# Kernel tuning notes

Hardware: AMD Instinct MI355X
Metric: run time of the kernel (lower is better)

Reference implementation:

```python
import jax, jax.numpy as jnp
import numpy as np

N_HEADS = 28
N_KV_HEADS = 4
HEAD_DIM = 128
ROPE_THETA = 1000000.0


def _sinusoidal_positions(num_pos, dim, theta):
    # Mirrors create_sinusoidal_positions: interleaved [sin, cos] pairs -> (num_pos, dim)
    positions = jnp.arange(0, num_pos, dtype=jnp.float32)
    half_dim = dim // 2
    freq_indices = jnp.arange(0, half_dim, dtype=jnp.float32)
    inv_freq = 1.0 / theta ** (freq_indices / half_dim)
    sinusoid_inp = jnp.einsum('i,j->ij', positions, inv_freq)
    return jnp.stack([jnp.sin(sinusoid_inp), jnp.cos(sinusoid_inp)], axis=-1).reshape(num_pos, -1)


def _rotate_half(x):
    x1, x2 = jnp.split(x, 2, axis=-1)
    return jnp.concatenate([-x2, x1], axis=-1)


def _apply_rope(q, k, sinu_pos):
    # Mirrors apply_rotary_pos_emb: split halves, duplicate, rotate_half mixing.
    sin, cos = jnp.split(sinu_pos, 2, axis=-1)
    sin = jnp.concatenate([sin, sin], axis=-1)[None, None, :, :]
    cos = jnp.concatenate([cos, cos], axis=-1)[None, None, :, :]
    q_embed = q * cos + _rotate_half(q) * sin
    k_embed = k * cos + _rotate_half(k) * sin
    return q_embed, k_embed


def setup_inputs() -> dict:
    key = jax.random.key(0)
    ks = jax.random.split(key, 5)
    B, S, H = 2, 2048, 3584
    std = 0.02
    return {
        'hidden_states': jax.random.normal(ks[0], (B, S, H), dtype=jnp.float32),
        'wq': jax.random.normal(ks[1], (H, N_HEADS * HEAD_DIM), dtype=jnp.float32) * std,
        'wk': jax.random.normal(ks[2], (H, N_KV_HEADS * HEAD_DIM), dtype=jnp.float32) * std,
        'wv': jax.random.normal(ks[3], (H, N_KV_HEADS * HEAD_DIM), dtype=jnp.float32) * std,
        'wo': jax.random.normal(ks[4], (N_HEADS * HEAD_DIM, H), dtype=jnp.float32) * std,
    }


def reference(hidden_states, wq, wk, wv, wo):
    B, S, H = hidden_states.shape
    gqa_ratio = N_HEADS // N_KV_HEADS

    # QKV projections (bias-free) and head split -> (B, heads, S, d)
    q = (hidden_states @ wq).reshape(B, S, N_HEADS, HEAD_DIM).transpose(0, 2, 1, 3)
    k = (hidden_states @ wk).reshape(B, S, N_KV_HEADS, HEAD_DIM).transpose(0, 2, 1, 3)
    v = (hidden_states @ wv).reshape(B, S, N_KV_HEADS, HEAD_DIM).transpose(0, 2, 1, 3)

    # Inline RoPE on Q/K
    sincos = _sinusoidal_positions(S, HEAD_DIM, ROPE_THETA)
    q, k = _apply_rope(q, k, sincos)

    # GQA head expansion via tile (matches jnp.tile in source: block-repeat)
    k = jnp.tile(k, (1, gqa_ratio, 1, 1))
    v = jnp.tile(v, (1, gqa_ratio, 1, 1))

    # Causal scaled dot-product attention
    scale = 1.0 / jnp.sqrt(jnp.float32(HEAD_DIM))
    scores = jnp.einsum('bhqd,bhkd->bhqk', q, k) * scale  # (B, H, S, S)
    causal = jnp.tril(jnp.ones((S, S), dtype=bool))
    scores = jnp.where(causal[None, None], scores, jnp.finfo(scores.dtype).min)
    probs = jax.nn.softmax(scores, axis=-1)
    out = jnp.einsum('bhqk,bhkd->bhqd', probs, v)

    # Merge heads and output projection
    out = out.transpose(0, 2, 1, 3).reshape(B, S, N_HEADS * HEAD_DIM)
    return out @ wo
```

## Files before the change

### kernel.cpp

```cpp
#include <hip/hip_runtime.h>
#include <hip/hip_bf16.h>

typedef __attribute__((ext_vector_type(4))) float f32x4;
typedef __attribute__((ext_vector_type(8))) short s16x8;
typedef __attribute__((ext_vector_type(4))) short s16x4;
typedef unsigned short u16;

__device__ __forceinline__ u16 f2bf(float f) {
  union { float f; unsigned int u; } v; v.f = f;
  unsigned int r = v.u + 0x7fffu + ((v.u >> 16) & 1u);
  return (u16)(r >> 16);
}
__device__ __forceinline__ float bf2f(u16 x) {
  union { unsigned u; float f; } v; v.u = ((unsigned)x) << 16; return v.f;
}

__device__ __forceinline__ void gload_lds16(const void* g, void* l) {
  __builtin_amdgcn_global_load_lds(
      (const __attribute__((address_space(1))) void*)g,
      (__attribute__((address_space(3))) void*)l, 16, 0, 0);
}

__global__ __launch_bounds__(256) void cvt_bf16(const float* __restrict__ in,
                                                u16* __restrict__ outp, int nquad) {
  int i = blockIdx.x * 256 + threadIdx.x;
  if (i >= nquad) return;
  f32x4 v = *(const f32x4*)(in + (size_t)i * 4);
  s16x4 o;
  o.x = (short)f2bf(v.x); o.y = (short)f2bf(v.y);
  o.z = (short)f2bf(v.z); o.w = (short)f2bf(v.w);
  *(s16x4*)(outp + (size_t)i * 4) = o;
}

__global__ __launch_bounds__(256) void transpose_cvt(const float* __restrict__ in,
                                                     u16* __restrict__ outp, int R, int C) {
  __shared__ float t[32][33];
  int c0 = blockIdx.x * 32, r0 = blockIdx.y * 32;
  int tx = threadIdx.x & 31, ty = threadIdx.x >> 5;
#pragma unroll
  for (int i = 0; i < 32; i += 8) t[ty + i][tx] = in[(size_t)(r0 + ty + i) * C + c0 + tx];
  __syncthreads();
#pragma unroll
  for (int i = 0; i < 32; i += 8)
    outp[(size_t)(c0 + ty + i) * R + r0 + tx] = f2bf(t[tx][ty + i]);
}

__global__ void rope_table(float2* __restrict__ tab) {
  int p = blockIdx.x, e = threadIdx.x;
  int j = e >> 1;
  float f1 = powf(1.0e6f, -(float)j / 64.0f);
  float f2 = powf(1.0e6f, -(float)(j + 32) / 64.0f);
  float a1 = (float)p * f1, a2 = (float)p * f2;
  float S = (e & 1) ? cosf(a1) : sinf(a1);
  float C = (e & 1) ? cosf(a2) : sinf(a2);
  tab[p * 64 + e] = make_float2(S, C);
}

__global__ __launch_bounds__(256) void rope_pack(const u16* __restrict__ P,
                                                 const float2* __restrict__ tab,
                                                 u16* __restrict__ outp, int nh, int ldp,
                                                 int coff, float scale) {
  int idx = blockIdx.x * 4 + (threadIdx.x >> 6);
  int e = threadIdx.x & 63;
  int s = idx & 2047;
  int bh = idx >> 11;
  int b = bh / nh, h = bh - b * nh;
  size_t prow = ((size_t)(b * 2048 + s)) * (size_t)ldp + coff + (size_t)h * 128;
  float x1 = bf2f(P[prow + e]), x2 = bf2f(P[prow + e + 64]);
  float2 t = tab[s * 64 + e];
  float o1 = (x1 * t.y - x2 * t.x) * scale;
  float o2 = (x2 * t.y + x1 * t.x) * scale;
  size_t orow = (size_t)idx * 128;
  outp[orow + e] = f2bf(o1);
  outp[orow + e + 64] = f2bf(o2);
}

__global__ __launch_bounds__(256) void pack_vt(const u16* __restrict__ P,
                                               u16* __restrict__ Vt, int ldp, int coff) {
  __shared__ u16 t[32][33];
  int bk = blockIdx.z;
  int b = bk >> 2, kh = bk & 3;
  int s0 = blockIdx.x * 32, d0 = blockIdx.y * 32;
  int tx = threadIdx.x & 31, ty = threadIdx.x >> 5;
  const u16* in = P + (size_t)(b * 2048) * ldp + coff + kh * 128;
#pragma unroll
  for (int i = 0; i < 32; i += 8) t[ty + i][tx] = in[(size_t)(s0 + ty + i) * ldp + d0 + tx];
  __syncthreads();
  u16* outp = Vt + (size_t)bk * 128 * 2048;
#pragma unroll
  for (int i = 0; i < 32; i += 8)
    outp[(size_t)(d0 + ty + i) * 2048 + s0 + tx] = t[tx][ty + i];
}

template <int OUT_BF16>
__global__ __launch_bounds__(512, 2) void gemm256(const u16* __restrict__ A,
                                                  const u16* __restrict__ BT,
                                                  void* __restrict__ Cv,
                                                  int M, int N, int K) {
  extern __shared__ u16 sm[];
  const int tid = threadIdx.x;
  const int lane = tid & 63, w = tid >> 6;
  const int wm = w >> 2, wn = w & 3;
  const int r = lane & 15, g = lane >> 4;
  const int bm = blockIdx.y * 256, bn = blockIdx.x * 256;

  f32x4 acc[8][4];
#pragma unroll
  for (int mf = 0; mf < 8; mf++)
#pragma unroll
    for (int nf = 0; nf < 4; nf++) acc[mf][nf] = (f32x4){0.f, 0.f, 0.f, 0.f};

  const int row_s = tid >> 3;
  const int col_s = ((((tid & 7) << 4) ^ ((row_s & 7) << 4)) >> 1);
  const u16* sAg[4]; const u16* sBg[4];
#pragma unroll
  for (int i = 0; i < 4; i++) {
    sAg[i] = A  + (size_t)(bm + i * 64 + row_s) * K + col_s;
    sBg[i] = BT + (size_t)(bn + i * 64 + row_s) * K + col_s;
  }

#pragma unroll
  for (int i = 0; i < 4; i++) gload_lds16(sAg[i], sm + i * 4096 + w * 512);
#pragma unroll
  for (int i = 0; i < 4; i++) gload_lds16(sBg[i], sm + 32768 + i * 4096 + w * 512);

  const int NT = K >> 6;
  const int swz = (r & 7) << 4;
#pragma unroll 1
  for (int t = 0; t < NT; ++t) {
    const int p = t & 1;
    const u16* LA = sm + p * 16384;
    const u16* LB = sm + 32768 + p * 16384;
    u16* SA = sm + (p ^ 1) * 16384;
    u16* SB = sm + 32768 + (p ^ 1) * 16384;
    const int ktn = (t + 1 < NT) ? (t + 1) * 64 : 0;

    __builtin_amdgcn_s_barrier();
    gload_lds16(sAg[0] + ktn, SA + 0 * 4096 + w * 512);
    gload_lds16(sAg[1] + ktn, SA + 1 * 4096 + w * 512);
    asm volatile("s_waitcnt vmcnt(2)" ::: "memory");
    __builtin_amdgcn_s_barrier();
    __builtin_amdgcn_sched_barrier(0);

    const char* Ac = (const char*)LA;
    const char* Bc = (const char*)LB;
    s16x8 bf[4][2];
#pragma unroll
    for (int nf = 0; nf < 4; nf++)
#pragma unroll
      for (int ks = 0; ks < 2; ks++) {
        int row = wn * 64 + nf * 16 + r;
        bf[nf][ks] = *(const s16x8*)(Bc + ((row * 128 + ks * 64 + g * 16) ^ swz));
      }
#pragma unroll
    for (int ph = 0; ph < 4; ph++) {
      if (ph == 1) {
        gload_lds16(sAg[2] + ktn, SA + 2 * 4096 + w * 512);
        gload_lds16(sAg[3] + ktn, SA + 3 * 4096 + w * 512);
      } else if (ph == 2) {
        gload_lds16(sBg[0] + ktn, SB + 0 * 4096 + w * 512);
        gload_lds16(sBg[1] + ktn, SB + 1 * 4096 + w * 512);
      } else if (ph == 3) {
        gload_lds16(sBg[2] + ktn, SB + 2 * 4096 + w * 512);
        gload_lds16(sBg[3] + ktn, SB + 3 * 4096 + w * 512);
      }
      s16x8 af[2][2];
#pragma unroll
      for (int mi = 0; mi < 2; mi++)
#pragma unroll
        for (int ks = 0; ks < 2; ks++) {
          int row = wm * 128 + (ph * 2 + mi) * 16 + r;
          af[mi][ks] = *(const s16x8*)(Ac + ((row * 128 + ks * 64 + g * 16) ^ swz));
        }
      __builtin_amdgcn_s_setprio(1);
#pragma unroll
      for (int mi = 0; mi < 2; mi++)
#pragma unroll
        for (int nf = 0; nf < 4; nf++) {
          acc[ph * 2 + mi][nf] = __builtin_amdgcn_mfma_f32_16x16x32_bf16(
              af[mi][0], bf[nf][0], acc[ph * 2 + mi][nf], 0, 0, 0);
          acc[ph * 2 + mi][nf] = __builtin_amdgcn_mfma_f32_16x16x32_bf16(
              af[mi][1], bf[nf][1], acc[ph * 2 + mi][nf], 0, 0, 0);
        }
      __builtin_amdgcn_s_setprio(0);
    }
  }
  asm volatile("s_waitcnt vmcnt(0)" ::: "memory");

#pragma unroll
  for (int mf = 0; mf < 8; mf++)
#pragma unroll
    for (int nf = 0; nf < 4; nf++)
#pragma unroll
      for (int jj = 0; jj < 4; jj++) {
        size_t idx = (size_t)(bm + wm * 128 + mf * 16 + g * 4 + jj) * N +
                     (bn + wn * 64 + nf * 16 + r);
        if constexpr (OUT_BF16) ((u16*)Cv)[idx] = f2bf(acc[mf][nf][jj]);
        else                    ((float*)Cv)[idx] = acc[mf][nf][jj];
      }
}

__global__ __launch_bounds__(256, 4) void attn_kernel(const u16* __restrict__ Q,
                                                      const u16* __restrict__ K,
                                                      const u16* __restrict__ Vt,
                                                      u16* __restrict__ AO) {
  constexpr int S = 2048, NH = 28, NKV = 4, D = 128;
  __shared__ u16 Kl[2][32 * 128];
  __shared__ u16 Vl[2][32 * 128];
  const int tid = threadIdx.x;
  const int lane = tid & 63, w = tid >> 6;
  const int r = lane & 15, g = lane >> 4;
  const int pp = blockIdx.x, h = blockIdx.y, b = blockIdx.z;
  const int kh = h & 3;
  const u16* Kb = K + ((size_t)(b * NKV + kh) * S) * D;
  const u16* Vb = Vt + ((size_t)(b * NKV + kh) * D) * S;

  const u16 *sK[2], *sV[2];
#pragma unroll
  for (int i = 0; i < 2; i++) {
    int o = i * 4096 + tid * 16;
    int krow = o >> 8;
    int kcol = ((o & 255) ^ ((krow & 7) << 4)) >> 1;
    sK[i] = Kb + (size_t)krow * D + kcol;
    int p = o ^ (((o >> 7) & 7) << 4);
    sV[i] = Vb + (size_t)(p >> 6) * S + ((p & 63) >> 1);
  }

#pragma unroll 1
  for (int seg = 0; seg < 2; ++seg) {
    const int qt = seg ? (31 - pp) : pp;
    const int q0 = qt * 64 + w * 16;
    const u16* Qb = Q + ((size_t)(b * NH + h) * S + q0) * D;

    s16x8 qf[4];
#pragma unroll
    for (int kb = 0; kb < 4; kb++)
      qf[kb] = *(const s16x8*)(Qb + (size_t)r * D + kb * 32 + g * 8);

    f32x4 o8[8];
#pragma unroll
    for (int c = 0; c < 8; c++) o8[c] = (f32x4){0.f, 0.f, 0.f, 0.f};
    float m = -1e30f, lsum = 0.f;
    const int qg = q0 + r;
    const int NT = 2 * qt + 2;

#pragma unroll
    for (int i = 0; i < 2; i++) {
      gload_lds16(sK[i], (u16*)Kl[0] + i * 2048 + tid * 8);
      gload_lds16(sV[i], (u16*)Vl[0] + i * 2048 + tid * 8);
    }

    int cur = 0;
#pragma unroll 1
    for (int t = 0; t < NT; ++t) {
      const int j = t * 32;
      if (t + 1 < NT) {
        const size_t jn = (size_t)(j + 32);
#pragma unroll
        for (int i = 0; i < 2; i++) {
          gload_lds16(sK[i] + jn * D, (u16*)Kl[cur ^ 1] + i * 2048 + tid * 8);
          gload_lds16(sV[i] + jn,     (u16*)Vl[cur ^ 1] + i * 2048 + tid * 8);
        }
        asm volatile("s_waitcnt vmcnt(4)" ::: "memory");
      } else {
        asm volatile("s_waitcnt vmcnt(0)" ::: "memory");
      }
      __builtin_amdgcn_s_barrier();
      __builtin_amdgcn_sched_barrier(0);
      if (j <= q0 + 15) {
        f32x4 st0 = (f32x4){0.f, 0.f, 0.f, 0.f};
        f32x4 st1 = (f32x4){0.f, 0.f, 0.f, 0.f};
        const int swz = (r & 7) << 4;
        const char* Kc = (const char*)Kl[cur];
        __builtin_amdgcn_s_setprio(1);
#pragma unroll
        for (int kb = 0; kb < 4; kb++) {
          int cb = (kb * 64 + g * 16) ^ swz;
          s16x8 kf = *(const s16x8*)(Kc + r * 256 + cb);
          st0 = __builtin_amdgcn_mfma_f32_16x16x32_bf16(kf, qf[kb], st0, 0, 0, 0);
        }
#pragma unroll
        for (int kb = 0; kb < 4; kb++) {
          int cb = (kb * 64 + g * 16) ^ swz;
          s16x8 kf = *(const s16x8*)(Kc + (r + 16) * 256 + cb);
          st1 = __builtin_amdgcn_mfma_f32_16x16x32_bf16(kf, qf[kb], st1, 0, 0, 0);
        }
        __builtin_amdgcn_s_setprio(0);
        float s8v[8];
        if (j + 31 <= q0) {
#pragma unroll
          for (int jj = 0; jj < 4; jj++) { s8v[jj] = st0[jj]; s8v[jj + 4] = st1[jj]; }
        } else {
#pragma unroll
          for (int jj = 0; jj < 4; jj++) {
            int kv0 = j + g * 4 + jj;
            s8v[jj] = (kv0 > qg) ? -1e30f : st0[jj];
            s8v[jj + 4] = (kv0 + 16 > qg) ? -1e30f : st1[jj];
          }
        }
        float pm = fmaxf(fmaxf(fmaxf(s8v[0], s8v[1]), fmaxf(s8v[2], s8v[3])),
                         fmaxf(fmaxf(s8v[4], s8v[5]), fmaxf(s8v[6], s8v[7])));
        const bool defer = __all(pm <= m + 8.f);
        float fr = 1.f;
        if (!defer) {
          pm = fmaxf(pm, __shfl_xor(pm, 16));
          pm = fmaxf(pm, __shfl_xor(pm, 32));
          float mnew = fmaxf(m, pm);
          fr = __expf(m - mnew);
          m = mnew;
        }
        float pv[8], psum = 0.f;
#pragma unroll
        for (int i2 = 0; i2 < 8; i2++) { pv[i2] = __expf(s8v[i2] - m); psum += pv[i2]; }
        lsum = lsum * fr + psum;
        unsigned pk[4];
#pragma unroll
        for (int i2 = 0; i2 < 4; i2++) {
          __hip_bfloat162 hv = __float22bfloat162_rn(make_float2(pv[2 * i2], pv[2 * i2 + 1]));
          union { __hip_bfloat162 h; unsigned u; } cv; cv.h = hv; pk[i2] = cv.u;
        }
        int L0 = r + ((g & 1) << 5);
        unsigned a0 = (unsigned)__shfl((int)pk[0], L0);
        unsigned a1 = (unsigned)__shfl((int)pk[1], L0);
        unsigned a2 = (unsigned)__shfl((int)pk[2], L0);
        unsigned a3 = (unsigned)__shfl((int)pk[3], L0);
        unsigned b0 = (unsigned)__shfl((int)pk[0], L0 + 16);
        unsigned b1 = (unsigned)__shfl((int)pk[1], L0 + 16);
        unsigned b2 = (unsigned)__shfl((int)pk[2], L0 + 16);
        unsigned b3 = (unsigned)__shfl((int)pk[3], L0 + 16);
        union { unsigned u[4]; s16x8 v; } pu;
        pu.u[0] = (g < 2) ? a0 : a2;
        pu.u[1] = (g < 2) ? a1 : a3;
        pu.u[2] = (g < 2) ? b0 : b2;
        pu.u[3] = (g < 2) ? b1 : b3;
        s16x8 pa = pu.v;
        float fB[4];
        if (!defer) {
#pragma unroll
          for (int jj = 0; jj < 4; jj++) fB[jj] = __shfl(fr, g * 4 + jj);
        }
        const char* Vc = (const char*)Vl[cur];
        __builtin_amdgcn_s_setprio(1);
#pragma unroll
        for (int c = 0; c < 8; c++) {
          int pbyte = (c * 16 + r) * 64 + g * 16;
          int vaddr = pbyte ^ ((r >> 1) << 4);
          s16x8 vf = *(const s16x8*)(Vc + vaddr);
          f32x4 oc = o8[c];
          if (!defer) { oc.x *= fB[0]; oc.y *= fB[1]; oc.z *= fB[2]; oc.w *= fB[3]; }
          o8[c] = __builtin_amdgcn_mfma_f32_16x16x32_bf16(pa, vf, oc, 0, 0, 0);
        }
        __builtin_amdgcn_s_setprio(0);
      }
      __builtin_amdgcn_s_barrier();
      cur ^= 1;
    }

    float lrow = lsum;
    lrow += __shfl_xor(lrow, 16);
    lrow += __shfl_xor(lrow, 32);
    float lB[4];
#pragma unroll
    for (int jj = 0; jj < 4; jj++) lB[jj] = __shfl(lrow, g * 4 + jj);
#pragma unroll
    for (int c = 0; c < 8; c++)
#pragma unroll
      for (int jj = 0; jj < 4; jj++) {
        float val = o8[c][jj] / lB[jj];
        AO[(size_t)(b * S + q0 + g * 4 + jj) * 3584 + h * 128 + c * 16 + r] = f2bf(val);
      }
  }
}

static const size_t OFF_XBF = 0;
static const size_t OFF_WQT = 29360128;
static const size_t OFF_WKT = 55050240;
static const size_t OFF_WVT = 58720256;
static const size_t OFF_WOT = 62390272;
static const size_t OFF_TAB = 88080384;
static const size_t OFF_QBF = 89128960;
static const size_t OFF_KBF = 118489088;
static const size_t OFF_VT  = 122683392;
static const size_t OFF_QKV = 126877696;
static const size_t OFF_AO  = 164626432;

extern "C" void kernel_launch(void* const* d_in, const int* in_sizes, int n_in,
                              void* d_out, int out_size, void* d_ws, size_t ws_size,
                              hipStream_t stream) {
  const float* X  = (const float*)d_in[0];
  const float* Wq = (const float*)d_in[1];
  const float* Wk = (const float*)d_in[2];
  const float* Wv = (const float*)d_in[3];
  const float* Wo = (const float*)d_in[4];
  float* out = (float*)d_out;
  char* ws = (char*)d_ws;

  u16* Xbf = (u16*)(ws + OFF_XBF);
  u16* WqT = (u16*)(ws + OFF_WQT);
  u16* WkT = (u16*)(ws + OFF_WKT);
  u16* WvT = (u16*)(ws + OFF_WVT);
  u16* WoT = (u16*)(ws + OFF_WOT);
  float2* tab = (float2*)(ws + OFF_TAB);
  u16* Qbf = (u16*)(ws + OFF_QBF);
  u16* Kbf = (u16*)(ws + OFF_KBF);
  u16* Vtb = (u16*)(ws + OFF_VT);
  u16* QKV = (u16*)(ws + OFF_QKV);
  u16* AO  = (u16*)(ws + OFF_AO);

  hipFuncSetAttribute(reinterpret_cast<const void*>(gemm256<1>),
                      hipFuncAttributeMaxDynamicSharedMemorySize, 131072);
  hipFuncSetAttribute(reinterpret_cast<const void*>(gemm256<0>),
                      hipFuncAttributeMaxDynamicSharedMemorySize, 131072);

  cvt_bf16<<<14336, 256, 0, stream>>>(X, Xbf, 3670016);
  transpose_cvt<<<dim3(112, 112), 256, 0, stream>>>(Wq, WqT, 3584, 3584);
  transpose_cvt<<<dim3(16, 112), 256, 0, stream>>>(Wk, WkT, 3584, 512);
  transpose_cvt<<<dim3(16, 112), 256, 0, stream>>>(Wv, WvT, 3584, 512);
  transpose_cvt<<<dim3(112, 112), 256, 0, stream>>>(Wo, WoT, 3584, 3584);
  rope_table<<<2048, 64, 0, stream>>>(tab);

  gemm256<1><<<dim3(18, 16), 512, 131072, stream>>>(Xbf, WqT, QKV, 4096, 4608, 3584);

  rope_pack<<<28672, 256, 0, stream>>>(QKV, tab, Qbf, 28, 4608, 0, 0.08838834764831845f);
  rope_pack<<<4096, 256, 0, stream>>>(QKV, tab, Kbf, 4, 4608, 3584, 1.0f);
  pack_vt<<<dim3(64, 4, 8), 256, 0, stream>>>(QKV, Vtb, 4608, 4096);

  attn_kernel<<<dim3(16, 28, 2), 256, 0, stream>>>(Qbf, Kbf, Vtb, AO);

  gemm256<0><<<dim3(14, 16), 512, 131072, stream>>>(AO, WoT, out, 4096, 3584, 3584);
}
```

Measured before the change: 510.2 us.

## Deepen GEMM prefetch to two stages and remap tiles per XCD

The 256x256 bf16 GEMM is restructured to prefetch the K-tile two iterations ahead, loading into the LDS buffer currently being consumed. Barriers are placed around each MFMA phase so loads can overwrite parts of the buffer once they have been read. Block IDs are also remapped so that blocks landing on the same XCD cover a contiguous rectangle of output tiles, which is meant to improve L2 reuse of A and B. The extra barriers per phase add synchronisation cost, and the in-place buffer reuse depends on the barrier placement being correct.

New measurement: 522.7 us. 1.02x slower.

```diff
diff --git a/kernel.cpp b/kernel.cpp
--- a/kernel.cpp
+++ b/kernel.cpp
@@ -96,13 +96,17 @@
 __global__ __launch_bounds__(512, 2) void gemm256(const u16* __restrict__ A,
                                                   const u16* __restrict__ BT,
                                                   void* __restrict__ Cv,
-                                                  int M, int N, int K) {
+                                                  int M, int N, int K,
+                                                  int CNX, int CNY, int XNX) {
   extern __shared__ u16 sm[];
   const int tid = threadIdx.x;
   const int lane = tid & 63, w = tid >> 6;
   const int wm = w >> 2, wn = w & 3;
   const int r = lane & 15, g = lane >> 4;
-  const int bm = blockIdx.y * 256, bn = blockIdx.x * 256;
+  const int lid = blockIdx.x;
+  const int xcd = lid & 7, pos = lid >> 3;
+  const int bn = ((xcd % XNX) * CNX + pos % CNX) * 256;
+  const int bm = ((xcd / XNX) * CNY + pos / CNX) * 256;
 
   f32x4 acc[8][4];
 #pragma unroll
@@ -120,49 +124,51 @@
   }
 
 #pragma unroll
-  for (int i = 0; i < 4; i++) gload_lds16(sAg[i], sm + i * 4096 + w * 512);
-#pragma unroll
   for (int i = 0; i < 4; i++) gload_lds16(sBg[i], sm + 32768 + i * 4096 + w * 512);
+  gload_lds16(sAg[0], sm + 0 * 4096 + w * 512);
+  gload_lds16(sAg[2], sm + 2 * 4096 + w * 512);
+  gload_lds16(sAg[1], sm + 1 * 4096 + w * 512);
+  gload_lds16(sAg[3], sm + 3 * 4096 + w * 512);
+#pragma unroll
+  for (int i = 0; i < 4; i++) gload_lds16(sBg[i] + 64, sm + 49152 + i * 4096 + w * 512);
+  gload_lds16(sAg[0] + 64, sm + 16384 + 0 * 4096 + w * 512);
+  gload_lds16(sAg[2] + 64, sm + 16384 + 2 * 4096 + w * 512);
+  gload_lds16(sAg[1] + 64, sm + 16384 + 1 * 4096 + w * 512);
+  gload_lds16(sAg[3] + 64, sm + 16384 + 3 * 4096 + w * 512);
+  asm volatile("s_waitcnt vmcnt(8)" ::: "memory");
+  __builtin_amdgcn_s_barrier();
 
   const int NT = K >> 6;
   const int swz = (r & 7) << 4;
 #pragma unroll 1
   for (int t = 0; t < NT; ++t) {
     const int p = t & 1;
-    const u16* LA = sm + p * 16384;
-    const u16* LB = sm + 32768 + p * 16384;
-    u16* SA = sm + (p ^ 1) * 16384;
-    u16* SB = sm + 32768 + (p ^ 1) * 16384;
-    const int ktn = (t + 1 < NT) ? (t + 1) * 64 : 0;
-
-    __builtin_amdgcn_s_barrier();
-    gload_lds16(sAg[0] + ktn, SA + 0 * 4096 + w * 512);
-    gload_lds16(sAg[1] + ktn, SA + 1 * 4096 + w * 512);
-    asm volatile("s_waitcnt vmcnt(2)" ::: "memory");
-    __builtin_amdgcn_s_barrier();
-    __builtin_amdgcn_sched_barrier(0);
-
-    const char* Ac = (const char*)LA;
-    const char* Bc = (const char*)LB;
+    const char* Ac = (const char*)(sm + p * 16384);
+    const char* Bc = (const char*)(sm + 32768 + p * 16384);
+    u16* SA = sm + p * 16384;
+    u16* SB = sm + 32768 + p * 16384;
+    const int kt2 = (t + 2 < NT) ? (t + 2) * 64 : 0;
+
     s16x8 bf[4][2];
-#pragma unroll
-    for (int nf = 0; nf < 4; nf++)
-#pragma unroll
-      for (int ks = 0; ks < 2; ks++) {
-        int row = wn * 64 + nf * 16 + r;
-        bf[nf][ks] = *(const s16x8*)(Bc + ((row * 128 + ks * 64 + g * 16) ^ swz));
-      }
 #pragma unroll
     for (int ph = 0; ph < 4; ph++) {
       if (ph == 1) {
-        gload_lds16(sAg[2] + ktn, SA + 2 * 4096 + w * 512);
-        gload_lds16(sAg[3] + ktn, SA + 3 * 4096 + w * 512);
+        gload_lds16(sBg[0] + kt2, SB + 0 * 4096 + w * 512);
+        gload_lds16(sBg[1] + kt2, SB + 1 * 4096 + w * 512);
+        gload_lds16(sBg[2] + kt2, SB + 2 * 4096 + w * 512);
+        gload_lds16(sBg[3] + kt2, SB + 3 * 4096 + w * 512);
       } else if (ph == 2) {
-        gload_lds16(sBg[0] + ktn, SB + 0 * 4096 + w * 512);
-        gload_lds16(sBg[1] + ktn, SB + 1 * 4096 + w * 512);
-      } else if (ph == 3) {
-        gload_lds16(sBg[2] + ktn, SB + 2 * 4096 + w * 512);
-        gload_lds16(sBg[3] + ktn, SB + 3 * 4096 + w * 512);
+        gload_lds16(sAg[0] + kt2, SA + 0 * 4096 + w * 512);
+        gload_lds16(sAg[2] + kt2, SA + 2 * 4096 + w * 512);
+      }
+      if (ph == 0) {
+#pragma unroll
+        for (int nf = 0; nf < 4; nf++)
+#pragma unroll
+          for (int ks = 0; ks < 2; ks++) {
+            int row = wn * 64 + nf * 16 + r;
+            bf[nf][ks] = *(const s16x8*)(Bc + ((row * 128 + ks * 64 + g * 16) ^ swz));
+          }
       }
       s16x8 af[2][2];
 #pragma unroll
@@ -172,6 +178,8 @@
           int row = wm * 128 + (ph * 2 + mi) * 16 + r;
           af[mi][ks] = *(const s16x8*)(Ac + ((row * 128 + ks * 64 + g * 16) ^ swz));
         }
+      __builtin_amdgcn_s_barrier();
+      __builtin_amdgcn_sched_barrier(0);
       __builtin_amdgcn_s_setprio(1);
 #pragma unroll
       for (int mi = 0; mi < 2; mi++)
@@ -183,7 +191,14 @@
               af[mi][1], bf[nf][1], acc[ph * 2 + mi][nf], 0, 0, 0);
         }
       __builtin_amdgcn_s_setprio(0);
+      __builtin_amdgcn_s_barrier();
+      __builtin_amdgcn_sched_barrier(0);
     }
+    gload_lds16(sAg[1] + kt2, SA + 1 * 4096 + w * 512);
+    gload_lds16(sAg[3] + kt2, SA + 3 * 4096 + w * 512);
+    asm volatile("s_waitcnt vmcnt(8)" ::: "memory");
+    __builtin_amdgcn_s_barrier();
+    __builtin_amdgcn_sched_barrier(0);
   }
   asm volatile("s_waitcnt vmcnt(0)" ::: "memory");
 
@@ -419,7 +434,7 @@
   transpose_cvt<<<dim3(112, 112), 256, 0, stream>>>(Wo, WoT, 3584, 3584);
   rope_table<<<2048, 64, 0, stream>>>(tab);
 
-  gemm256<1><<<dim3(18, 16), 512, 131072, stream>>>(Xbf, WqT, QKV, 4096, 4608, 3584);
+  gemm256<1><<<288, 512, 131072, stream>>>(Xbf, WqT, QKV, 4096, 4608, 3584, 9, 4, 2);
 
   rope_pack<<<28672, 256, 0, stream>>>(QKV, tab, Qbf, 28, 4608, 0, 0.08838834764831845f);
   rope_pack<<<4096, 256, 0, stream>>>(QKV, tab, Kbf, 4, 4608, 3584, 1.0f);
@@ -427,5 +442,5 @@
 
   attn_kernel<<<dim3(16, 28, 2), 256, 0, stream>>>(Qbf, Kbf, Vtb, AO);
 
-  gemm256<0><<<dim3(14, 16), 512, 131072, stream>>>(AO, WoT, out, 4096, 3584, 3584);
-}
+  gemm256<0><<<224, 512, 131072, stream>>>(AO, WoT, out, 4096, 3584, 3584, 7, 4, 2);
+}
```

## Remap GEMM tiles per XCD and restructure double-buffered load pipeline

Applied to the files above, without the earlier changes.

Switches the GEMM grid to a 1D launch and maps block IDs so that each of the 8 XCDs gets a contiguous rectangular group of output tiles, which should improve L2 reuse of A and B panels. The K-loop prefetch is reordered so B tiles load first and A tiles later. Explicit vmcnt waits and barriers now bracket each MFMA phase, replacing the single barrier pair at the top of each iteration. This adds more barriers per iteration, and the mapping assumes round-robin dispatch of blocks across XCDs.

Result: slower. 521.0 us (+2.1%).

```diff
diff --git a/kernel.cpp b/kernel.cpp
--- a/kernel.cpp
+++ b/kernel.cpp
@@ -96,13 +96,17 @@
 __global__ __launch_bounds__(512, 2) void gemm256(const u16* __restrict__ A,
                                                   const u16* __restrict__ BT,
                                                   void* __restrict__ Cv,
-                                                  int M, int N, int K) {
+                                                  int M, int N, int K,
+                                                  int CNX, int CNY, int XNX) {
   extern __shared__ u16 sm[];
   const int tid = threadIdx.x;
   const int lane = tid & 63, w = tid >> 6;
   const int wm = w >> 2, wn = w & 3;
   const int r = lane & 15, g = lane >> 4;
-  const int bm = blockIdx.y * 256, bn = blockIdx.x * 256;
+  const int lid = blockIdx.x;
+  const int xcd = lid & 7, pos = lid >> 3;
+  const int bn = ((xcd % XNX) * CNX + pos % CNX) * 256;
+  const int bm = ((xcd / XNX) * CNY + pos / CNX) * 256;
 
   f32x4 acc[8][4];
 #pragma unroll
@@ -120,49 +124,51 @@
   }
 
 #pragma unroll
-  for (int i = 0; i < 4; i++) gload_lds16(sAg[i], sm + i * 4096 + w * 512);
-#pragma unroll
   for (int i = 0; i < 4; i++) gload_lds16(sBg[i], sm + 32768 + i * 4096 + w * 512);
+  gload_lds16(sAg[0], sm + 0 * 4096 + w * 512);
+  gload_lds16(sAg[2], sm + 2 * 4096 + w * 512);
+  gload_lds16(sAg[1], sm + 1 * 4096 + w * 512);
+  gload_lds16(sAg[3], sm + 3 * 4096 + w * 512);
+  asm volatile("s_waitcnt vmcnt(2)" ::: "memory");
+  __builtin_amdgcn_s_barrier();
 
   const int NT = K >> 6;
   const int swz = (r & 7) << 4;
 #pragma unroll 1
   for (int t = 0; t < NT; ++t) {
     const int p = t & 1;
-    const u16* LA = sm + p * 16384;
-    const u16* LB = sm + 32768 + p * 16384;
+    const char* Ac = (const char*)(sm + p * 16384);
+    const char* Bc = (const char*)(sm + 32768 + p * 16384);
     u16* SA = sm + (p ^ 1) * 16384;
     u16* SB = sm + 32768 + (p ^ 1) * 16384;
     const int ktn = (t + 1 < NT) ? (t + 1) * 64 : 0;
 
-    __builtin_amdgcn_s_barrier();
-    gload_lds16(sAg[0] + ktn, SA + 0 * 4096 + w * 512);
-    gload_lds16(sAg[1] + ktn, SA + 1 * 4096 + w * 512);
-    asm volatile("s_waitcnt vmcnt(2)" ::: "memory");
-    __builtin_amdgcn_s_barrier();
-    __builtin_amdgcn_sched_barrier(0);
-
-    const char* Ac = (const char*)LA;
-    const char* Bc = (const char*)LB;
     s16x8 bf[4][2];
 #pragma unroll
-    for (int nf = 0; nf < 4; nf++)
-#pragma unroll
-      for (int ks = 0; ks < 2; ks++) {
-        int row = wn * 64 + nf * 16 + r;
-        bf[nf][ks] = *(const s16x8*)(Bc + ((row * 128 + ks * 64 + g * 16) ^ swz));
-      }
-#pragma unroll
     for (int ph = 0; ph < 4; ph++) {
-      if (ph == 1) {
-        gload_lds16(sAg[2] + ktn, SA + 2 * 4096 + w * 512);
-        gload_lds16(sAg[3] + ktn, SA + 3 * 4096 + w * 512);
-      } else if (ph == 2) {
+      if (ph == 0) {
         gload_lds16(sBg[0] + ktn, SB + 0 * 4096 + w * 512);
         gload_lds16(sBg[1] + ktn, SB + 1 * 4096 + w * 512);
-      } else if (ph == 3) {
+      } else if (ph == 1) {
         gload_lds16(sBg[2] + ktn, SB + 2 * 4096 + w * 512);
         gload_lds16(sBg[3] + ktn, SB + 3 * 4096 + w * 512);
+        asm volatile("s_waitcnt vmcnt(4)" ::: "memory");
+      } else if (ph == 2) {
+        gload_lds16(sAg[0] + ktn, SA + 0 * 4096 + w * 512);
+        gload_lds16(sAg[2] + ktn, SA + 2 * 4096 + w * 512);
+      } else {
+        gload_lds16(sAg[1] + ktn, SA + 1 * 4096 + w * 512);
+        gload_lds16(sAg[3] + ktn, SA + 3 * 4096 + w * 512);
+        asm volatile("s_waitcnt vmcnt(2)" ::: "memory");
+      }
+      if (ph == 0) {
+#pragma unroll
+        for (int nf = 0; nf < 4; nf++)
+#pragma unroll
+          for (int ks = 0; ks < 2; ks++) {
+            int row = wn * 64 + nf * 16 + r;
+            bf[nf][ks] = *(const s16x8*)(Bc + ((row * 128 + ks * 64 + g * 16) ^ swz));
+          }
       }
       s16x8 af[2][2];
 #pragma unroll
@@ -172,6 +178,7 @@
           int row = wm * 128 + (ph * 2 + mi) * 16 + r;
           af[mi][ks] = *(const s16x8*)(Ac + ((row * 128 + ks * 64 + g * 16) ^ swz));
         }
+      __builtin_amdgcn_s_barrier();
       __builtin_amdgcn_s_setprio(1);
 #pragma unroll
       for (int mi = 0; mi < 2; mi++)
@@ -183,6 +190,7 @@
               af[mi][1], bf[nf][1], acc[ph * 2 + mi][nf], 0, 0, 0);
         }
       __builtin_amdgcn_s_setprio(0);
+      __builtin_amdgcn_s_barrier();
     }
   }
   asm volatile("s_waitcnt vmcnt(0)" ::: "memory");
@@ -419,7 +427,7 @@
   transpose_cvt<<<dim3(112, 112), 256, 0, stream>>>(Wo, WoT, 3584, 3584);
   rope_table<<<2048, 64, 0, stream>>>(tab);
 
-  gemm256<1><<<dim3(18, 16), 512, 131072, stream>>>(Xbf, WqT, QKV, 4096, 4608, 3584);
+  gemm256<1><<<288, 512, 131072, stream>>>(Xbf, WqT, QKV, 4096, 4608, 3584, 9, 4, 2);
 
   rope_pack<<<28672, 256, 0, stream>>>(QKV, tab, Qbf, 28, 4608, 0, 0.08838834764831845f);
   rope_pack<<<4096, 256, 0, stream>>>(QKV, tab, Kbf, 4, 4608, 3584, 1.0f);
@@ -427,5 +435,5 @@
 
   attn_kernel<<<dim3(16, 28, 2), 256, 0, stream>>>(Qbf, Kbf, Vtb, AO);
 
-  gemm256<0><<<dim3(14, 16), 512, 131072, stream>>>(AO, WoT, out, 4096, 3584, 3584);
-}
+  gemm256<0><<<224, 512, 131072, stream>>>(AO, WoT, out, 4096, 3584, 3584, 7, 4, 2);
+}
```

## Replace 256x256 GEMM with 128x128 tile kernel for better CU fill

Applied to the files above, without the earlier changes.

Swaps the 512-thread, 256x256-tile GEMM (128KB dynamic LDS, K-step 64) for a 256-thread 128x128-tile kernel with 32KB static LDS, a K-step of 32 and a simple double buffer. Both the QKV and output projections now launch several times as many blocks. This is meant to fix poor wave quantisation: the output projection previously ran only 224 blocks on a 256-CU device. The cost is less data reuse per tile, more global and LDS traffic, and more barriers per K-iteration. The attention output buffer now reuses the QKV workspace region.

Result: slower. 550.2 us (+7.8%).

```diff
diff --git a/kernel.cpp b/kernel.cpp
--- a/kernel.cpp
+++ b/kernel.cpp
@@ -92,111 +92,87 @@
     outp[(size_t)(d0 + ty + i) * 2048 + s0 + tx] = t[tx][ty + i];
 }
 
-template <int OUT_BF16>
-__global__ __launch_bounds__(512, 2) void gemm256(const u16* __restrict__ A,
+__global__ __launch_bounds__(256, 3) void gemm128(const u16* __restrict__ A,
                                                   const u16* __restrict__ BT,
                                                   void* __restrict__ Cv,
-                                                  int M, int N, int K) {
-  extern __shared__ u16 sm[];
+                                                  int M, int N, int K, int obf16) {
+  __shared__ u16 sm[16384];
   const int tid = threadIdx.x;
-  const int lane = tid & 63, w = tid >> 6;
-  const int wm = w >> 2, wn = w & 3;
+  const int lane = tid & 63, wave = tid >> 6;
+  const int bm = blockIdx.y * 128, bn = blockIdx.x * 128;
+  const int wr = (wave >> 1) * 64, wc = (wave & 1) * 64;
   const int r = lane & 15, g = lane >> 4;
-  const int bm = blockIdx.y * 256, bn = blockIdx.x * 256;
-
-  f32x4 acc[8][4];
-#pragma unroll
-  for (int mf = 0; mf < 8; mf++)
-#pragma unroll
-    for (int nf = 0; nf < 4; nf++) acc[mf][nf] = (f32x4){0.f, 0.f, 0.f, 0.f};
-
-  const int row_s = tid >> 3;
-  const int col_s = ((((tid & 7) << 4) ^ ((row_s & 7) << 4)) >> 1);
-  const u16* sAg[4]; const u16* sBg[4];
-#pragma unroll
-  for (int i = 0; i < 4; i++) {
-    sAg[i] = A  + (size_t)(bm + i * 64 + row_s) * K + col_s;
-    sBg[i] = BT + (size_t)(bn + i * 64 + row_s) * K + col_s;
+
+  f32x4 acc[4][4];
+#pragma unroll
+  for (int i = 0; i < 4; i++)
+#pragma unroll
+    for (int j = 0; j < 4; j++) acc[i][j] = (f32x4){0.f, 0.f, 0.f, 0.f};
+
+  const u16 *srcA[2], *srcB[2];
+#pragma unroll
+  for (int i = 0; i < 2; i++) {
+    int row = i * 64 + (tid >> 2);
+    int cb = ((tid & 3) * 16) ^ (((row >> 1) & 3) << 4);
+    srcA[i] = A  + (size_t)(bm + row) * K + (cb >> 1);
+    srcB[i] = BT + (size_t)(bn + row) * K + (cb >> 1);
   }
 
 #pragma unroll
-  for (int i = 0; i < 4; i++) gload_lds16(sAg[i], sm + i * 4096 + w * 512);
-#pragma unroll
-  for (int i = 0; i < 4; i++) gload_lds16(sBg[i], sm + 32768 + i * 4096 + w * 512);
-
-  const int NT = K >> 6;
-  const int swz = (r & 7) << 4;
+  for (int i = 0; i < 2; i++) gload_lds16(srcA[i], sm + i * 2048 + tid * 8);
+#pragma unroll
+  for (int i = 0; i < 2; i++) gload_lds16(srcB[i], sm + 8192 + i * 2048 + tid * 8);
+
+  const int NT = K >> 5;
 #pragma unroll 1
   for (int t = 0; t < NT; ++t) {
     const int p = t & 1;
-    const u16* LA = sm + p * 16384;
-    const u16* LB = sm + 32768 + p * 16384;
-    u16* SA = sm + (p ^ 1) * 16384;
-    u16* SB = sm + 32768 + (p ^ 1) * 16384;
-    const int ktn = (t + 1 < NT) ? (t + 1) * 64 : 0;
-
+    const char* Ac = (const char*)(sm + p * 4096);
+    const char* Bc = (const char*)(sm + 8192 + p * 4096);
+    if (t + 1 < NT) {
+      const int ktn = (t + 1) * 32;
+      u16* SA = sm + (p ^ 1) * 4096;
+      u16* SB = sm + 8192 + (p ^ 1) * 4096;
+#pragma unroll
+      for (int i = 0; i < 2; i++) gload_lds16(srcA[i] + ktn, SA + i * 2048 + tid * 8);
+#pragma unroll
+      for (int i = 0; i < 2; i++) gload_lds16(srcB[i] + ktn, SB + i * 2048 + tid * 8);
+      asm volatile("s_waitcnt vmcnt(4)" ::: "memory");
+    } else {
+      asm volatile("s_waitcnt vmcnt(0)" ::: "memory");
+    }
     __builtin_amdgcn_s_barrier();
-    gload_lds16(sAg[0] + ktn, SA + 0 * 4096 + w * 512);
-    gload_lds16(sAg[1] + ktn, SA + 1 * 4096 + w * 512);
-    asm volatile("s_waitcnt vmcnt(2)" ::: "memory");
+
+    s16x8 af[4], bf[4];
+#pragma unroll
+    for (int mf = 0; mf < 4; mf++) {
+      int row = wr + mf * 16 + r;
+      af[mf] = *(const s16x8*)(Ac + row * 64 + ((g * 16) ^ (((row >> 1) & 3) << 4)));
+    }
+#pragma unroll
+    for (int nf = 0; nf < 4; nf++) {
+      int row = wc + nf * 16 + r;
+      bf[nf] = *(const s16x8*)(Bc + row * 64 + ((g * 16) ^ (((row >> 1) & 3) << 4)));
+    }
+    __builtin_amdgcn_s_setprio(1);
+#pragma unroll
+    for (int mf = 0; mf < 4; mf++)
+#pragma unroll
+      for (int nf = 0; nf < 4; nf++)
+        acc[mf][nf] = __builtin_amdgcn_mfma_f32_16x16x32_bf16(af[mf], bf[nf], acc[mf][nf], 0, 0, 0);
+    __builtin_amdgcn_s_setprio(0);
     __builtin_amdgcn_s_barrier();
-    __builtin_amdgcn_sched_barrier(0);
-
-    const char* Ac = (const char*)LA;
-    const char* Bc = (const char*)LB;
-    s16x8 bf[4][2];
+  }
+
+#pragma unroll
+  for (int mf = 0; mf < 4; mf++)
 #pragma unroll
     for (int nf = 0; nf < 4; nf++)
 #pragma unroll
-      for (int ks = 0; ks < 2; ks++) {
-        int row = wn * 64 + nf * 16 + r;
-        bf[nf][ks] = *(const s16x8*)(Bc + ((row * 128 + ks * 64 + g * 16) ^ swz));
-      }
-#pragma unroll
-    for (int ph = 0; ph < 4; ph++) {
-      if (ph == 1) {
-        gload_lds16(sAg[2] + ktn, SA + 2 * 4096 + w * 512);
-        gload_lds16(sAg[3] + ktn, SA + 3 * 4096 + w * 512);
-      } else if (ph == 2) {
-        gload_lds16(sBg[0] + ktn, SB + 0 * 4096 + w * 512);
-        gload_lds16(sBg[1] + ktn, SB + 1 * 4096 + w * 512);
-      } else if (ph == 3) {
-        gload_lds16(sBg[2] + ktn, SB + 2 * 4096 + w * 512);
-        gload_lds16(sBg[3] + ktn, SB + 3 * 4096 + w * 512);
-      }
-      s16x8 af[2][2];
-#pragma unroll
-      for (int mi = 0; mi < 2; mi++)
-#pragma unroll
-        for (int ks = 0; ks < 2; ks++) {
-          int row = wm * 128 + (ph * 2 + mi) * 16 + r;
-          af[mi][ks] = *(const s16x8*)(Ac + ((row * 128 + ks * 64 + g * 16) ^ swz));
-        }
-      __builtin_amdgcn_s_setprio(1);
-#pragma unroll
-      for (int mi = 0; mi < 2; mi++)
-#pragma unroll
-        for (int nf = 0; nf < 4; nf++) {
-          acc[ph * 2 + mi][nf] = __builtin_amdgcn_mfma_f32_16x16x32_bf16(
-              af[mi][0], bf[nf][0], acc[ph * 2 + mi][nf], 0, 0, 0);
-          acc[ph * 2 + mi][nf] = __builtin_amdgcn_mfma_f32_16x16x32_bf16(
-              af[mi][1], bf[nf][1], acc[ph * 2 + mi][nf], 0, 0, 0);
-        }
-      __builtin_amdgcn_s_setprio(0);
-    }
-  }
-  asm volatile("s_waitcnt vmcnt(0)" ::: "memory");
-
-#pragma unroll
-  for (int mf = 0; mf < 8; mf++)
-#pragma unroll
-    for (int nf = 0; nf < 4; nf++)
-#pragma unroll
       for (int jj = 0; jj < 4; jj++) {
-        size_t idx = (size_t)(bm + wm * 128 + mf * 16 + g * 4 + jj) * N +
-                     (bn + wn * 64 + nf * 16 + r);
-        if constexpr (OUT_BF16) ((u16*)Cv)[idx] = f2bf(acc[mf][nf][jj]);
-        else                    ((float*)Cv)[idx] = acc[mf][nf][jj];
+        size_t idx = (size_t)(bm + wr + mf * 16 + g * 4 + jj) * N + (bn + wc + nf * 16 + r);
+        if (obf16) ((u16*)Cv)[idx] = f2bf(acc[mf][nf][jj]);
+        else       ((float*)Cv)[idx] = acc[mf][nf][jj];
       }
 }
 
@@ -382,7 +358,6 @@
 static const size_t OFF_KBF = 118489088;
 static const size_t OFF_VT  = 122683392;
 static const size_t OFF_QKV = 126877696;
-static const size_t OFF_AO  = 164626432;
 
 extern "C" void kernel_launch(void* const* d_in, const int* in_sizes, int n_in,
                               void* d_out, int out_size, void* d_ws, size_t ws_size,
@@ -405,12 +380,7 @@
   u16* Kbf = (u16*)(ws + OFF_KBF);
   u16* Vtb = (u16*)(ws + OFF_VT);
   u16* QKV = (u16*)(ws + OFF_QKV);
-  u16* AO  = (u16*)(ws + OFF_AO);
-
-  hipFuncSetAttribute(reinterpret_cast<const void*>(gemm256<1>),
-                      hipFuncAttributeMaxDynamicSharedMemorySize, 131072);
-  hipFuncSetAttribute(reinterpret_cast<const void*>(gemm256<0>),
-                      hipFuncAttributeMaxDynamicSharedMemorySize, 131072);
+  u16* AO  = (u16*)(ws + OFF_QKV);
 
   cvt_bf16<<<14336, 256, 0, stream>>>(X, Xbf, 3670016);
   transpose_cvt<<<dim3(112, 112), 256, 0, stream>>>(Wq, WqT, 3584, 3584);
@@ -419,7 +389,7 @@
   transpose_cvt<<<dim3(112, 112), 256, 0, stream>>>(Wo, WoT, 3584, 3584);
   rope_table<<<2048, 64, 0, stream>>>(tab);
 
-  gemm256<1><<<dim3(18, 16), 512, 131072, stream>>>(Xbf, WqT, QKV, 4096, 4608, 3584);
+  gemm128<<<dim3(36, 32), 256, 0, stream>>>(Xbf, WqT, QKV, 4096, 4608, 3584, 1);
 
   rope_pack<<<28672, 256, 0, stream>>>(QKV, tab, Qbf, 28, 4608, 0, 0.08838834764831845f);
   rope_pack<<<4096, 256, 0, stream>>>(QKV, tab, Kbf, 4, 4608, 3584, 1.0f);
@@ -427,5 +397,5 @@
 
   attn_kernel<<<dim3(16, 28, 2), 256, 0, stream>>>(Qbf, Kbf, Vtb, AO);
 
-  gemm256<0><<<dim3(14, 16), 512, 131072, stream>>>(AO, WoT, out, 4096, 3584, 3584);
-}
+  gemm128<<<dim3(28, 32), 256, 0, stream>>>(AO, WoT, out, 4096, 3584, 3584, 0);
+}
```
